# Optimization experiments

Hardware: AMD Instinct MI355X
Metric: run time of the kernel (lower is better)

## Reference

```python
import jax, jax.numpy as jnp
import numpy as np

B, N, D, H, F = 2, 2048, 1024, 16, 4096
E = D // H
EPS = 1e-5

def layer_norm(x, g, b):
    mu = jnp.mean(x, axis=-1, keepdims=True)
    var = jnp.var(x, axis=-1, keepdims=True)
    return (x - mu) * jax.lax.rsqrt(var + EPS) * g + b

def setup_inputs() -> dict:
    key = jax.random.key(0)
    ks = jax.random.split(key, 16)
    s = lambda k, sh, fan: jax.random.normal(k, sh, jnp.float32) * (1.0 / np.sqrt(fan))
    return {
        'x': jax.random.normal(ks[0], (B, N, D), jnp.float32),
        'wq': s(ks[1], (D, D), D), 'bq': jnp.zeros((D,), jnp.float32),
        'wk': s(ks[2], (D, D), D), 'bk': jnp.zeros((D,), jnp.float32),
        'wv': s(ks[3], (D, D), D), 'bv': jnp.zeros((D,), jnp.float32),
        'w1': s(ks[4], (F, D), D), 'b1': jnp.zeros((F,), jnp.float32),
        'ln_mlp_g': jnp.ones((F,), jnp.float32), 'ln_mlp_b': jnp.zeros((F,), jnp.float32),
        'w2': s(ks[5], (D, F), F), 'b2': jnp.zeros((D,), jnp.float32),
        'ln1_g': jnp.ones((D,), jnp.float32), 'ln1_b': jnp.zeros((D,), jnp.float32),
        'ln2_g': jnp.ones((D,), jnp.float32), 'ln2_b': jnp.zeros((D,), jnp.float32),
    }

def reference(x, wq, bq, wk, bk, wv, bv, w1, b1, ln_mlp_g, ln_mlp_b, w2, b2, ln1_g, ln1_b, ln2_g, ln2_b):
    h = layer_norm(x, ln1_g, ln1_b)                       # [B,N,D]
    q = (h @ wq.T + bq).reshape(B, N, H, E).transpose(0, 2, 1, 3)  # [B,H,N,E]
    k = (h @ wk.T + bk).reshape(B, N, H, E).transpose(0, 2, 1, 3)
    v = (h @ wv.T + bv).reshape(B, N, H, E).transpose(0, 2, 1, 3)
    # faithful to source: score = q@k^T / sqrt(1/emb_dim) == q@k^T * sqrt(emb_dim)
    score = jnp.einsum('bhne,bhme->bhnm', q, k) * np.sqrt(D).astype(np.float32)
    causal = jnp.tril(jnp.ones((N, N), bool))
    score = jnp.where(causal[None, None], score, -jnp.inf)
    weight = jax.nn.softmax(score, axis=-1)
    attn = jnp.einsum('bhnm,bhme->bhne', weight, v)       # [B,H,N,E]
    attn = attn.transpose(0, 2, 1, 3).reshape(B, N, D)
    x = x + attn
    h2 = layer_norm(x, ln2_g, ln2_b)
    m = h2 @ w1.T + b1                                    # [B,N,F]
    m = jax.nn.relu(layer_norm(m, ln_mlp_g, ln_mlp_b))
    # faithful: no second residual in the source forward
    return m @ w2.T + b2
```

## Files before the change

kernel.cpp:

```cpp
#include <hip/hip_runtime.h>
#include <cstdint>

typedef __bf16 bf16_t;
typedef bf16_t bf16x8 __attribute__((ext_vector_type(8)));
typedef bf16_t bf16x4 __attribute__((ext_vector_type(4)));
typedef float  floatx4 __attribute__((ext_vector_type(4)));

#define GLD_LDS(g, l) __builtin_amdgcn_global_load_lds( \
    (const __attribute__((address_space(1))) unsigned int*)(g), \
    (__attribute__((address_space(3))) unsigned int*)(l), 16, 0, 0)

#define MFMA_BF16_16x16x32 __builtin_amdgcn_mfma_f32_16x16x32_bf16

__global__ __launch_bounds__(256) void prep(
    const float* __restrict__ wq, const float* __restrict__ wk,
    const float* __restrict__ wv, const float* __restrict__ w1,
    const float* __restrict__ w2, const float* __restrict__ bq,
    const float* __restrict__ bk,
    bf16_t* __restrict__ wqk_hi, bf16_t* __restrict__ wqk_lo,
    bf16_t* __restrict__ wvb, bf16_t* __restrict__ w1b, bf16_t* __restrict__ w2b,
    float* __restrict__ bqk) {
  const int blk = blockIdx.x, tid = threadIdx.x;
  if (blk < 2048) {
    const int qk = blk >> 10;
    const int i  = (blk & 1023) * 256 + tid;
    const float* src = qk ? wk : wq;
    float4 v = ((const float4*)src)[i];
    float f[4] = {v.x, v.y, v.z, v.w};
    bf16x4 h, l;
    #pragma unroll
    for (int j = 0; j < 4; ++j) { h[j] = (bf16_t)f[j]; l[j] = (bf16_t)(f[j] - (float)h[j]); }
    ((bf16x4*)(wqk_hi + qk * 1024 * 1024))[i] = h;
    ((bf16x4*)(wqk_lo + qk * 1024 * 1024))[i] = l;
  } else if (blk < 3072) {
    const int i = (blk - 2048) * 256 + tid;
    float4 v = ((const float4*)wv)[i];
    bf16x4 o; o[0]=(bf16_t)v.x; o[1]=(bf16_t)v.y; o[2]=(bf16_t)v.z; o[3]=(bf16_t)v.w;
    ((bf16x4*)wvb)[i] = o;
  } else if (blk < 7168) {
    const int i = (blk - 3072) * 256 + tid;
    float4 v = ((const float4*)w1)[i];
    bf16x4 o; o[0]=(bf16_t)v.x; o[1]=(bf16_t)v.y; o[2]=(bf16_t)v.z; o[3]=(bf16_t)v.w;
    ((bf16x4*)w1b)[i] = o;
  } else if (blk < 11264) {
    const int i = (blk - 7168) * 256 + tid;
    float4 v = ((const float4*)w2)[i];
    bf16x4 o; o[0]=(bf16_t)v.x; o[1]=(bf16_t)v.y; o[2]=(bf16_t)v.z; o[3]=(bf16_t)v.w;
    ((bf16x4*)w2b)[i] = o;
  } else {
    const int i = (blk - 11264) * 256 + tid;
    if (i < 1024) { bqk[i] = bq[i]; bqk[1024 + i] = bk[i]; }
  }
}


__device__ __forceinline__ void block_sum2(float& s, float& ss, float* red) {
  #pragma unroll
  for (int off = 32; off > 0; off >>= 1) {
    s  += __shfl_down(s, off);
    ss += __shfl_down(ss, off);
  }
  const int wave = threadIdx.x >> 6;
  if ((threadIdx.x & 63) == 0) { red[wave * 2] = s; red[wave * 2 + 1] = ss; }
  __syncthreads();
  s  = red[0] + red[2] + red[4] + red[6];
  ss = red[1] + red[3] + red[5] + red[7];
}

__global__ __launch_bounds__(256) void ln_fwd_split(const float* __restrict__ x,
    const float* __restrict__ g, const float* __restrict__ b,
    bf16_t* __restrict__ out_hi, bf16_t* __restrict__ out_lo) {
  __shared__ float red[8];
  const size_t row = blockIdx.x;
  float4 v = ((const float4*)(x + row * 1024))[threadIdx.x];
  float s  = v.x + v.y + v.z + v.w;
  float ss = v.x*v.x + v.y*v.y + v.z*v.z + v.w*v.w;
  block_sum2(s, ss, red);
  const float mu  = s * (1.f / 1024.f);
  const float var = ss * (1.f / 1024.f) - mu * mu;
  const float rs  = rsqrtf(var + 1e-5f);
  float4 gg = ((const float4*)g)[threadIdx.x];
  float4 bb = ((const float4*)b)[threadIdx.x];
  float f[4];
  f[0] = (v.x - mu) * rs * gg.x + bb.x;
  f[1] = (v.y - mu) * rs * gg.y + bb.y;
  f[2] = (v.z - mu) * rs * gg.z + bb.z;
  f[3] = (v.w - mu) * rs * gg.w + bb.w;
  bf16x4 oh, ol;
  #pragma unroll
  for (int j = 0; j < 4; ++j) {
    oh[j] = (bf16_t)f[j];
    ol[j] = (bf16_t)(f[j] - (float)oh[j]);
  }
  ((bf16x4*)(out_hi + row * 1024))[threadIdx.x] = oh;
  ((bf16x4*)(out_lo + row * 1024))[threadIdx.x] = ol;
}

__global__ __launch_bounds__(256) void resid_ln_fwd(const float* __restrict__ x,
    const float* __restrict__ a, const float* __restrict__ g, const float* __restrict__ b,
    bf16_t* __restrict__ out) {
  __shared__ float red[8];
  const size_t row = blockIdx.x;
  float4 v = ((const float4*)(x + row * 1024))[threadIdx.x];
  float4 av = ((const float4*)(a + row * 1024))[threadIdx.x];
  v.x += av.x; v.y += av.y; v.z += av.z; v.w += av.w;
  float s  = v.x + v.y + v.z + v.w;
  float ss = v.x*v.x + v.y*v.y + v.z*v.z + v.w*v.w;
  block_sum2(s, ss, red);
  const float mu  = s * (1.f / 1024.f);
  const float var = ss * (1.f / 1024.f) - mu * mu;
  const float rs  = rsqrtf(var + 1e-5f);
  float4 gg = ((const float4*)g)[threadIdx.x];
  float4 bb = ((const float4*)b)[threadIdx.x];
  bf16x4 o;
  o[0] = (bf16_t)((v.x - mu) * rs * gg.x + bb.x);
  o[1] = (bf16_t)((v.y - mu) * rs * gg.y + bb.y);
  o[2] = (bf16_t)((v.z - mu) * rs * gg.z + bb.z);
  o[3] = (bf16_t)((v.w - mu) * rs * gg.w + bb.w);
  ((bf16x4*)(out + row * 1024))[threadIdx.x] = o;
}

__global__ __launch_bounds__(256) void ln_relu_inplace(bf16_t* __restrict__ m,
    const float* __restrict__ g, const float* __restrict__ b) {
  __shared__ float red[8];
  const size_t row = blockIdx.x;
  bf16_t* mr = m + row * 4096;
  const int base = threadIdx.x * 16;
  bf16x8 v0 = *(bf16x8*)(mr + base);
  bf16x8 v1 = *(bf16x8*)(mr + base + 8);
  float f[16];
  #pragma unroll
  for (int i = 0; i < 8; ++i) { f[i] = (float)v0[i]; f[8 + i] = (float)v1[i]; }
  float s = 0.f, ss = 0.f;
  #pragma unroll
  for (int i = 0; i < 16; ++i) { s += f[i]; ss += f[i] * f[i]; }
  block_sum2(s, ss, red);
  const float mu  = s * (1.f / 4096.f);
  const float var = ss * (1.f / 4096.f) - mu * mu;
  const float rs  = rsqrtf(var + 1e-5f);
  bf16x8 o0, o1;
  #pragma unroll
  for (int i = 0; i < 16; ++i) {
    float ov = (f[i] - mu) * rs * g[base + i] + b[base + i];
    ov = fmaxf(ov, 0.f);
    if (i < 8) o0[i] = (bf16_t)ov; else o1[i - 8] = (bf16_t)ov;
  }
  *(bf16x8*)(mr + base) = o0;
  *(bf16x8*)(mr + base + 8) = o1;
}

template <int OUT_MODE, int BM>
__global__ __launch_bounds__(256) void gemm_bt(
    const bf16_t* __restrict__ A, const bf16_t* __restrict__ Bw,
    const float* __restrict__ bias, void* __restrict__ Cp,
    int M, int N, int K) {
  constexpr int MI = BM / 32;
  __shared__ bf16_t As[BM * 32];
  __shared__ bf16_t Bs[128 * 32];
  const int tid  = threadIdx.x;
  const int wave = tid >> 6, lane = tid & 63;
  const int quad = lane >> 4, l15 = lane & 15;
  const int m0 = blockIdx.x * BM, n0 = blockIdx.y * 128;
  const int wm = (wave >> 1) * (BM / 2), wn = (wave & 1) * 64;
  const int srowA = wave * (BM / 4) + (lane >> 2);
  const int srowB = wave * 32 + (lane >> 2);
  const int scol = (lane & 3) * 8;

  floatx4 acc[MI][4] = {};

  const bf16_t* Ag = A  + (size_t)(m0 + srowA) * K + scol;
  const bf16_t* Bg = Bw + (size_t)(n0 + srowB) * K + scol;

  for (int k0 = 0; k0 < K; k0 += 32) {
    __syncthreads();
    #pragma unroll
    for (int i = 0; i < BM / 64; ++i)
      GLD_LDS(Ag + (size_t)(i * 16) * K + k0, As + wave * (BM / 4) * 32 + i * 512);
    #pragma unroll
    for (int i = 0; i < 2; ++i)
      GLD_LDS(Bg + (size_t)(i * 16) * K + k0, Bs + wave * 1024 + i * 512);
    __syncthreads();
    bf16x8 af[MI], bfr[4];
    #pragma unroll
    for (int i = 0; i < MI; ++i)
      af[i] = *(const bf16x8*)(As + (wm + i * 16 + l15) * 32 + quad * 8);
    #pragma unroll
    for (int j = 0; j < 4; ++j)
      bfr[j] = *(const bf16x8*)(Bs + (wn + j * 16 + l15) * 32 + quad * 8);
    #pragma unroll
    for (int i = 0; i < MI; ++i)
      #pragma unroll
      for (int j = 0; j < 4; ++j)
        acc[i][j] = MFMA_BF16_16x16x32(af[i], bfr[j], acc[i][j], 0, 0, 0);
  }
  #pragma unroll
  for (int j = 0; j < 4; ++j) {
    const int col = n0 + wn + j * 16 + l15;
    const float bv = bias[col];
    #pragma unroll
    for (int i = 0; i < MI; ++i) {
      #pragma unroll
      for (int r = 0; r < 4; ++r) {
        const int row = m0 + wm + i * 16 + quad * 4 + r;
        const float v = acc[i][j][r] + bv;
        if (OUT_MODE == 0) {
          ((float*)Cp)[(size_t)row * N + col] = v;
        } else if (OUT_MODE == 1) {
          ((bf16_t*)Cp)[(size_t)row * N + col] = (bf16_t)v;
        } else {
          const int b = row >> 11, n = row & 2047;
          const int h = col >> 6, e = col & 63;
          ((bf16_t*)Cp)[(((size_t)((b << 4) + h) * 2048 + n) << 6) + e] = (bf16_t)v;
        }
      }
    }
  }
}

__global__ __launch_bounds__(256) void gemm_qk_split(
    const bf16_t* __restrict__ Ah, const bf16_t* __restrict__ Al,
    const bf16_t* __restrict__ Bh, const bf16_t* __restrict__ Bl,
    const float* __restrict__ bias,
    bf16_t* __restrict__ qhi, bf16_t* __restrict__ qlo,
    bf16_t* __restrict__ khi, bf16_t* __restrict__ klo,
    int M, int N, int K) {
  __shared__ bf16_t Ash[64 * 32];
  __shared__ bf16_t Asl[64 * 32];
  __shared__ bf16_t Bsh[128 * 32];
  __shared__ bf16_t Bsl[128 * 32];
  const int tid  = threadIdx.x;
  const int wave = tid >> 6, lane = tid & 63;
  const int quad = lane >> 4, l15 = lane & 15;
  const int m0 = blockIdx.x * 64, n0 = blockIdx.y * 128;
  const int wm = (wave >> 1) * 32, wn = (wave & 1) * 64;
  const int srowA = wave * 16 + (lane >> 2);
  const int srowB = wave * 32 + (lane >> 2);
  const int scol = (lane & 3) * 8;

  floatx4 acc[2][4] = {};

  const size_t aoff = (size_t)(m0 + srowA) * K + scol;
  const size_t boff = (size_t)(n0 + srowB) * K + scol;

  for (int k0 = 0; k0 < K; k0 += 32) {
    __syncthreads();
    GLD_LDS(Ah + aoff + k0, Ash + wave * 512);
    GLD_LDS(Al + aoff + k0, Asl + wave * 512);
    #pragma unroll
    for (int i = 0; i < 2; ++i) {
      const size_t gb = boff + (size_t)(i * 16) * K + k0;
      GLD_LDS(Bh + gb, Bsh + wave * 1024 + i * 512);
      GLD_LDS(Bl + gb, Bsl + wave * 1024 + i * 512);
    }
    __syncthreads();
    bf16x8 ah[2], al[2], bh[4], bl[4];
    #pragma unroll
    for (int i = 0; i < 2; ++i) {
      const int ro = (wm + i * 16 + l15) * 32 + quad * 8;
      ah[i] = *(const bf16x8*)(Ash + ro);
      al[i] = *(const bf16x8*)(Asl + ro);
    }
    #pragma unroll
    for (int j = 0; j < 4; ++j) {
      const int ro = (wn + j * 16 + l15) * 32 + quad * 8;
      bh[j] = *(const bf16x8*)(Bsh + ro);
      bl[j] = *(const bf16x8*)(Bsl + ro);
    }
    #pragma unroll
    for (int i = 0; i < 2; ++i)
      #pragma unroll
      for (int j = 0; j < 4; ++j) {
        acc[i][j] = MFMA_BF16_16x16x32(ah[i], bh[j], acc[i][j], 0, 0, 0);
        acc[i][j] = MFMA_BF16_16x16x32(ah[i], bl[j], acc[i][j], 0, 0, 0);
        acc[i][j] = MFMA_BF16_16x16x32(al[i], bh[j], acc[i][j], 0, 0, 0);
      }
  }
  #pragma unroll
  for (int j = 0; j < 4; ++j) {
    const int col = n0 + wn + j * 16 + l15;
    const float bv = bias[col];
    const bool isq = col < 1024;
    bf16_t* hib = isq ? qhi : khi;
    bf16_t* lob = isq ? qlo : klo;
    const float scale = isq ? 32.0f : 1.0f;
    const int h = (col >> 6) & 15, e = col & 63;
    #pragma unroll
    for (int i = 0; i < 2; ++i) {
      #pragma unroll
      for (int r = 0; r < 4; ++r) {
        const int row = m0 + wm + i * 16 + quad * 4 + r;
        const int b = row >> 11, n = row & 2047;
        const float c = (acc[i][j][r] + bv) * scale;
        const bf16_t chi = (bf16_t)c;
        const bf16_t clo = (bf16_t)(c - (float)chi);
        const size_t dst = (((size_t)((b << 4) + h) * 2048 + n) << 6) + e;
        hib[dst] = chi;
        lob[dst] = clo;
      }
    }
  }
}

__global__ __launch_bounds__(256) void transpose_v(
    const bf16_t* __restrict__ vhm, bf16_t* __restrict__ vT) {
  __shared__ bf16_t T[64 * 72];
  const int bh = blockIdx.x, n0 = blockIdx.y * 64;
  const int r = threadIdx.x >> 2;
  const int c = (threadIdx.x & 3) * 16;
  const bf16_t* src = vhm + ((size_t)bh * 2048 + n0 + r) * 64 + c;
  bf16x8 a0 = *(const bf16x8*)src;
  bf16x8 a1 = *(const bf16x8*)(src + 8);
  #pragma unroll
  for (int j = 0; j < 8; ++j) {
    T[(c + j) * 72 + r]     = a0[j];
    T[(c + 8 + j) * 72 + r] = a1[j];
  }
  __syncthreads();
  bf16x8 o0 = *(const bf16x8*)(T + r * 72 + c);
  bf16x8 o1 = *(const bf16x8*)(T + r * 72 + c + 8);
  bf16_t* dst = vT + ((size_t)(bh * 64 + r)) * 2048 + n0 + c;
  *(bf16x8*)dst = o0;
  *(bf16x8*)(dst + 8) = o1;
}

__global__ __launch_bounds__(256, 4) void attn_causal(
    const bf16_t* __restrict__ qhi, const bf16_t* __restrict__ qlo,
    const bf16_t* __restrict__ khi, const bf16_t* __restrict__ klo,
    const bf16_t* __restrict__ vT, float* __restrict__ o) {
  __shared__ bf16_t KsH[64 * 72];
  __shared__ bf16_t KsL[64 * 72];
  __shared__ bf16_t Vt[64 * 72];
  __shared__ bf16_t Ps[4][16 * 70];

  const int tid  = threadIdx.x;
  const int wave = tid >> 6, lane = tid & 63;
  const int quad = lane >> 4, l15 = lane & 15;
  const int bh = blockIdx.x;
  const int q0 = (31 - (int)blockIdx.y) * 64;
  const size_t hb = (size_t)bh * 2048;

  const int wmin = q0 + wave * 16;
  const int qrow = wmin + l15;
  bf16x8 qh[2], ql[2];
  {
    const bf16_t* qbh = qhi + ((hb + wmin + l15) << 6) + quad * 8;
    const bf16_t* qbl = qlo + ((hb + wmin + l15) << 6) + quad * 8;
    qh[0] = *(const bf16x8*)qbh;
    qh[1] = *(const bf16x8*)(qbh + 32);
    ql[0] = *(const bf16x8*)qbl;
    ql[1] = *(const bf16x8*)(qbl + 32);
  }

  floatx4 accO[4] = {};
  float m_row = -1e30f;
  float l_row = 0.f;

  const int kr = wave * 16 + (lane >> 3);
  const int kc = (lane & 7) * 8;
  const bf16_t* kgh = khi + ((hb + kr) << 6) + kc;
  const bf16_t* kgl = klo + ((hb + kr) << 6) + kc;
  const bf16_t* vg  = vT + ((size_t)(bh * 64 + kr)) * 2048 + kc;

  bf16x8 pkh0 = *(const bf16x8*)(kgh);
  bf16x8 pkh1 = *(const bf16x8*)(kgh + (8 << 6));
  bf16x8 pkl0 = *(const bf16x8*)(kgl);
  bf16x8 pkl1 = *(const bf16x8*)(kgl + (8 << 6));
  bf16x8 pv0  = *(const bf16x8*)(vg);
  bf16x8 pv1  = *(const bf16x8*)(vg + 8 * 2048);

  const int ntiles = (q0 >> 6) + 1;
  for (int t = 0; t < ntiles; ++t) {
    const int k0 = t * 64;
    __syncthreads();
    *(bf16x8*)(KsH + kr * 72 + kc)       = pkh0;
    *(bf16x8*)(KsH + (kr + 8) * 72 + kc) = pkh1;
    *(bf16x8*)(KsL + kr * 72 + kc)       = pkl0;
    *(bf16x8*)(KsL + (kr + 8) * 72 + kc) = pkl1;
    *(bf16x8*)(Vt  + kr * 72 + kc)       = pv0;
    *(bf16x8*)(Vt  + (kr + 8) * 72 + kc) = pv1;
    if (t + 1 < ntiles) {
      const int koff = (t + 1) << 12;
      pkh0 = *(const bf16x8*)(kgh + koff);
      pkh1 = *(const bf16x8*)(kgh + koff + (8 << 6));
      pkl0 = *(const bf16x8*)(kgl + koff);
      pkl1 = *(const bf16x8*)(kgl + koff + (8 << 6));
      pv0  = *(const bf16x8*)(vg + (t + 1) * 64);
      pv1  = *(const bf16x8*)(vg + (t + 1) * 64 + 8 * 2048);
    }
    __syncthreads();

    const bool needmask = (k0 + 63 > wmin);

    floatx4 sv[4];
    #pragma unroll
    for (int j = 0; j < 4; ++j) {
      const bf16_t* kbh = KsH + (j * 16 + l15) * 72;
      const bf16_t* kbl = KsL + (j * 16 + l15) * 72;
      const bf16x8 kh0 = *(const bf16x8*)(kbh + quad * 8);
      const bf16x8 kh1 = *(const bf16x8*)(kbh + 32 + quad * 8);
      const bf16x8 kl0 = *(const bf16x8*)(kbl + quad * 8);
      const bf16x8 kl1 = *(const bf16x8*)(kbl + 32 + quad * 8);
      floatx4 acc = {};
      acc = MFMA_BF16_16x16x32(kh0, qh[0], acc, 0, 0, 0);
      acc = MFMA_BF16_16x16x32(kh1, qh[1], acc, 0, 0, 0);
      acc = MFMA_BF16_16x16x32(kl0, qh[0], acc, 0, 0, 0);
      acc = MFMA_BF16_16x16x32(kl1, qh[1], acc, 0, 0, 0);
      acc = MFMA_BF16_16x16x32(kh0, ql[0], acc, 0, 0, 0);
      acc = MFMA_BF16_16x16x32(kh1, ql[1], acc, 0, 0, 0);
      sv[j] = acc;
    }

    const int lim = qrow - k0 - quad * 4;
    float mr = -1e30f;
    #pragma unroll
    for (int j = 0; j < 4; ++j)
      #pragma unroll
      for (int r = 0; r < 4; ++r) {
        float x = sv[j][r];
        if (needmask && (j * 16 + r > lim)) x = -1e30f;
        sv[j][r] = x;
        mr = fmaxf(mr, x);
      }
    mr = fmaxf(mr, __shfl_xor(mr, 16));
    mr = fmaxf(mr, __shfl_xor(mr, 32));
    const float mold = m_row;
    const float mnew = fmaxf(mold, mr);
    m_row = mnew;
    float psum = 0.f;
    bf16x4 pb[4];
    #pragma unroll
    for (int j = 0; j < 4; ++j)
      #pragma unroll
      for (int r = 0; r < 4; ++r) {
        const float p = __expf(sv[j][r] - mnew);
        const bf16_t pv = (bf16_t)p;
        psum += (float)pv;
        pb[j][r] = pv;
      }
    {
      bf16_t* pw = &Ps[wave][l15 * 70];
      #pragma unroll
      for (int j = 0; j < 4; ++j)
        *(bf16x4*)(pw + j * 16 + quad * 4) = pb[j];
    }
    psum += __shfl_xor(psum, 16);
    psum += __shfl_xor(psum, 32);
    const float alpha = __expf(mold - mnew);
    l_row = l_row * alpha + psum;
    if (__any(mnew > mold)) {
      #pragma unroll
      for (int r = 0; r < 4; ++r) {
        const float ar = __shfl(alpha, quad * 4 + r);
        #pragma unroll
        for (int j = 0; j < 4; ++j) accO[j][r] *= ar;
      }
    }
    asm volatile("s_waitcnt lgkmcnt(0)" ::: "memory");

    bf16x8 pf[2];
    {
      const bf16_t* pr = &Ps[wave][l15 * 70];
      pf[0] = *(const bf16x8*)(pr + quad * 8);
      pf[1] = *(const bf16x8*)(pr + 32 + quad * 8);
    }
    #pragma unroll
    for (int j = 0; j < 4; ++j) {
      const bf16_t* vb = Vt + (j * 16 + l15) * 72;
      const bf16x8 vf0 = *(const bf16x8*)(vb + quad * 8);
      const bf16x8 vf1 = *(const bf16x8*)(vb + 32 + quad * 8);
      accO[j] = MFMA_BF16_16x16x32(pf[0], vf0, accO[j], 0, 0, 0);
      accO[j] = MFMA_BF16_16x16x32(pf[1], vf1, accO[j], 0, 0, 0);
    }
  }

  const int b = bh >> 4, h = bh & 15;
  #pragma unroll
  for (int r = 0; r < 4; ++r) {
    const float lr = __shfl(l_row, quad * 4 + r);
    const float linv = 1.f / lr;
    const int qr = wmin + quad * 4 + r;
    float* orow = o + ((size_t)(b * 2048) + qr) * 1024 + h * 64;
    #pragma unroll
    for (int j = 0; j < 4; ++j)
      orow[j * 16 + l15] = accO[j][r] * linv;
  }
}


extern "C" void kernel_launch(void* const* d_in, const int* in_sizes, int n_in,
                              void* d_out, int out_size, void* d_ws, size_t ws_size,
                              hipStream_t stream) {
  const float* x        = (const float*)d_in[0];
  const float* wq       = (const float*)d_in[1];
  const float* bq       = (const float*)d_in[2];
  const float* wk       = (const float*)d_in[3];
  const float* bk       = (const float*)d_in[4];
  const float* wv       = (const float*)d_in[5];
  const float* bv       = (const float*)d_in[6];
  const float* w1       = (const float*)d_in[7];
  const float* b1       = (const float*)d_in[8];
  const float* ln_mlp_g = (const float*)d_in[9];
  const float* ln_mlp_b = (const float*)d_in[10];
  const float* w2       = (const float*)d_in[11];
  const float* b2       = (const float*)d_in[12];
  const float* ln1_g    = (const float*)d_in[13];
  const float* ln1_b    = (const float*)d_in[14];
  const float* ln2_g    = (const float*)d_in[15];
  const float* ln2_b    = (const float*)d_in[16];

  char* ws = (char*)d_ws;
  bf16_t* h_hi   = (bf16_t*)(ws);
  bf16_t* h_lo   = (bf16_t*)(ws + (8u  << 20));
  bf16_t* vTb    = (bf16_t*)(ws);
  bf16_t* wqk_hi = (bf16_t*)(ws + (16u << 20));
  bf16_t* wqk_lo = (bf16_t*)(ws + (20u << 20));
  bf16_t* wvb    = (bf16_t*)(ws + (24u << 20));
  float*  bqk    = (float*) (ws + (26u << 20));
  bf16_t* w1b    = (bf16_t*)(ws + (28u << 20));
  bf16_t* w2b    = (bf16_t*)(ws + (36u << 20));
  bf16_t* qhi    = (bf16_t*)(ws + (44u << 20));
  bf16_t* qlo    = (bf16_t*)(ws + (52u << 20));
  bf16_t* khi    = (bf16_t*)(ws + (60u << 20));
  bf16_t* klo    = (bf16_t*)(ws + (68u << 20));
  bf16_t* mbuf   = (bf16_t*)(ws + (44u << 20));
  bf16_t* vhm    = (bf16_t*)(ws + (76u << 20));
  float*  attnb  = (float*) (ws + (84u << 20));
  bf16_t* h2     = (bf16_t*)(ws + (100u << 20));

  prep<<<11268, 256, 0, stream>>>(wq, wk, wv, w1, w2, bq, bk,
                                  wqk_hi, wqk_lo, wvb, w1b, w2b, bqk);

  ln_fwd_split<<<4096, 256, 0, stream>>>(x, ln1_g, ln1_b, h_hi, h_lo);
  gemm_qk_split<<<dim3(64, 16), 256, 0, stream>>>(h_hi, h_lo, wqk_hi, wqk_lo, bqk,
                                                  qhi, qlo, khi, klo, 4096, 2048, 1024);
  gemm_bt<2, 64><<<dim3(64, 8), 256, 0, stream>>>(h_hi, wvb, bv, vhm, 4096, 1024, 1024);
  transpose_v<<<dim3(32, 32), 256, 0, stream>>>(vhm, vTb);
  attn_causal<<<dim3(32, 32), 256, 0, stream>>>(qhi, qlo, khi, klo, vTb, attnb);
  resid_ln_fwd<<<4096, 256, 0, stream>>>(x, attnb, ln2_g, ln2_b, h2);
  gemm_bt<1, 128><<<dim3(32, 32), 256, 0, stream>>>(h2, w1b, b1, mbuf, 4096, 4096, 1024);
  ln_relu_inplace<<<4096, 256, 0, stream>>>(mbuf, ln_mlp_g, ln_mlp_b);
  gemm_bt<0, 64><<<dim3(64, 8), 256, 0, stream>>>(mbuf, w2b, b2, d_out, 4096, 1024, 4096);

  (void)in_sizes; (void)n_in; (void)out_size; (void)ws_size;
}
```

Baseline: 472.8 us.

## Swizzle attention LDS layout, add XCD block remap and MFMA priority hints

Replaces the padded LDS tiles in the attention kernel with XOR-swizzled unpadded layouts. This cuts shared memory per block and raises the occupancy hint from 4 to 5 blocks. It also adds an XCD-aware block index remap to the GEMM kernels to improve L2 locality, and wraps the attention MFMA sections in s_setprio plus a sched_barrier. The swizzle must keep bank conflicts low, and the remap assumes the grid size divides evenly by 8.

```diff
diff --git a/kernel.cpp b/kernel.cpp
--- a/kernel.cpp
+++ b/kernel.cpp
@@ -149,6 +149,15 @@
   *(bf16x8*)(mr + base + 8) = o1;
 }
 
+__device__ __forceinline__ void xcd_swizzle(int& bx, int& by) {
+  const int gx = gridDim.x;
+  const int nwg = gx * gridDim.y;
+  const int flat = by * gx + bx;
+  const int cpx = nwg >> 3;
+  const int swz = (flat & 7) * cpx + (flat >> 3);
+  bx = swz % gx; by = swz / gx;
+}
+
 template <int OUT_MODE, int BM>
 __global__ __launch_bounds__(256) void gemm_bt(
     const bf16_t* __restrict__ A, const bf16_t* __restrict__ Bw,
@@ -160,7 +169,9 @@
   const int tid  = threadIdx.x;
   const int wave = tid >> 6, lane = tid & 63;
   const int quad = lane >> 4, l15 = lane & 15;
-  const int m0 = blockIdx.x * BM, n0 = blockIdx.y * 128;
+  int bx = blockIdx.x, by = blockIdx.y;
+  xcd_swizzle(bx, by);
+  const int m0 = bx * BM, n0 = by * 128;
   const int wm = (wave >> 1) * (BM / 2), wn = (wave & 1) * 64;
   const int srowA = wave * (BM / 4) + (lane >> 2);
   const int srowB = wave * 32 + (lane >> 2);
@@ -231,7 +242,9 @@
   const int tid  = threadIdx.x;
   const int wave = tid >> 6, lane = tid & 63;
   const int quad = lane >> 4, l15 = lane & 15;
-  const int m0 = blockIdx.x * 64, n0 = blockIdx.y * 128;
+  int bx = blockIdx.x, by = blockIdx.y;
+  xcd_swizzle(bx, by);
+  const int m0 = bx * 64, n0 = by * 128;
   const int wm = (wave >> 1) * 32, wn = (wave & 1) * 64;
   const int srowA = wave * 16 + (lane >> 2);
   const int srowB = wave * 32 + (lane >> 2);
@@ -323,14 +336,15 @@
   *(bf16x8*)(dst + 8) = o1;
 }
 
-__global__ __launch_bounds__(256, 4) void attn_causal(
+#define SWZ(row, chunk) (((row) << 6) + ((((chunk) ^ ((row) & 7))) << 3))
+__global__ __launch_bounds__(256, 5) void attn_causal(
     const bf16_t* __restrict__ qhi, const bf16_t* __restrict__ qlo,
     const bf16_t* __restrict__ khi, const bf16_t* __restrict__ klo,
     const bf16_t* __restrict__ vT, float* __restrict__ o) {
-  __shared__ bf16_t KsH[64 * 72];
-  __shared__ bf16_t KsL[64 * 72];
-  __shared__ bf16_t Vt[64 * 72];
-  __shared__ bf16_t Ps[4][16 * 70];
+  __shared__ bf16_t KsH[64 * 64];
+  __shared__ bf16_t KsL[64 * 64];
+  __shared__ bf16_t Vt[64 * 64];
+  __shared__ bf16_t Ps[4][16 * 64];
 
   const int tid  = threadIdx.x;
   const int wave = tid >> 6, lane = tid & 63;
@@ -356,10 +370,10 @@
   float l_row = 0.f;
 
   const int kr = wave * 16 + (lane >> 3);
-  const int kc = (lane & 7) * 8;
-  const bf16_t* kgh = khi + ((hb + kr) << 6) + kc;
-  const bf16_t* kgl = klo + ((hb + kr) << 6) + kc;
-  const bf16_t* vg  = vT + ((size_t)(bh * 64 + kr)) * 2048 + kc;
+  const int kc7 = lane & 7;
+  const bf16_t* kgh = khi + ((hb + kr) << 6) + kc7 * 8;
+  const bf16_t* kgl = klo + ((hb + kr) << 6) + kc7 * 8;
+  const bf16_t* vg  = vT + ((size_t)(bh * 64 + kr)) * 2048 + kc7 * 8;
 
   bf16x8 pkh0 = *(const bf16x8*)(kgh);
   bf16x8 pkh1 = *(const bf16x8*)(kgh + (8 << 6));
@@ -372,12 +386,12 @@
   for (int t = 0; t < ntiles; ++t) {
     const int k0 = t * 64;
     __syncthreads();
-    *(bf16x8*)(KsH + kr * 72 + kc)       = pkh0;
-    *(bf16x8*)(KsH + (kr + 8) * 72 + kc) = pkh1;
-    *(bf16x8*)(KsL + kr * 72 + kc)       = pkl0;
-    *(bf16x8*)(KsL + (kr + 8) * 72 + kc) = pkl1;
-    *(bf16x8*)(Vt  + kr * 72 + kc)       = pv0;
-    *(bf16x8*)(Vt  + (kr + 8) * 72 + kc) = pv1;
+    *(bf16x8*)(KsH + SWZ(kr, kc7))     = pkh0;
+    *(bf16x8*)(KsH + SWZ(kr + 8, kc7)) = pkh1;
+    *(bf16x8*)(KsL + SWZ(kr, kc7))     = pkl0;
+    *(bf16x8*)(KsL + SWZ(kr + 8, kc7)) = pkl1;
+    *(bf16x8*)(Vt  + SWZ(kr, kc7))     = pv0;
+    *(bf16x8*)(Vt  + SWZ(kr + 8, kc7)) = pv1;
     if (t + 1 < ntiles) {
       const int koff = (t + 1) << 12;
       pkh0 = *(const bf16x8*)(kgh + koff);
@@ -392,14 +406,14 @@
     const bool needmask = (k0 + 63 > wmin);
 
     floatx4 sv[4];
+    __builtin_amdgcn_s_setprio(1);
     #pragma unroll
     for (int j = 0; j < 4; ++j) {
-      const bf16_t* kbh = KsH + (j * 16 + l15) * 72;
-      const bf16_t* kbl = KsL + (j * 16 + l15) * 72;
-      const bf16x8 kh0 = *(const bf16x8*)(kbh + quad * 8);
-      const bf16x8 kh1 = *(const bf16x8*)(kbh + 32 + quad * 8);
-      const bf16x8 kl0 = *(const bf16x8*)(kbl + quad * 8);
-      const bf16x8 kl1 = *(const bf16x8*)(kbl + 32 + quad * 8);
+      const int rK = j * 16 + l15;
+      const bf16x8 kh0 = *(const bf16x8*)(KsH + SWZ(rK, quad));
+      const bf16x8 kh1 = *(const bf16x8*)(KsH + SWZ(rK, quad + 4));
+      const bf16x8 kl0 = *(const bf16x8*)(KsL + SWZ(rK, quad));
+      const bf16x8 kl1 = *(const bf16x8*)(KsL + SWZ(rK, quad + 4));
       floatx4 acc = {};
       acc = MFMA_BF16_16x16x32(kh0, qh[0], acc, 0, 0, 0);
       acc = MFMA_BF16_16x16x32(kh1, qh[1], acc, 0, 0, 0);
@@ -409,6 +423,7 @@
       acc = MFMA_BF16_16x16x32(kh1, ql[1], acc, 0, 0, 0);
       sv[j] = acc;
     }
+    __builtin_amdgcn_s_setprio(0);
 
     const int lim = qrow - k0 - quad * 4;
     float mr = -1e30f;
@@ -438,10 +453,10 @@
         pb[j][r] = pv;
       }
     {
-      bf16_t* pw = &Ps[wave][l15 * 70];
+      bf16_t* pw = &Ps[wave][0];
       #pragma unroll
       for (int j = 0; j < 4; ++j)
-        *(bf16x4*)(pw + j * 16 + quad * 4) = pb[j];
+        *(bf16x4*)(pw + SWZ(l15, 2 * j + (quad >> 1)) + (quad & 1) * 4) = pb[j];
     }
     psum += __shfl_xor(psum, 16);
     psum += __shfl_xor(psum, 32);
@@ -456,21 +471,24 @@
       }
     }
     asm volatile("s_waitcnt lgkmcnt(0)" ::: "memory");
+    __builtin_amdgcn_sched_barrier(0);
 
     bf16x8 pf[2];
     {
-      const bf16_t* pr = &Ps[wave][l15 * 70];
-      pf[0] = *(const bf16x8*)(pr + quad * 8);
-      pf[1] = *(const bf16x8*)(pr + 32 + quad * 8);
-    }
+      const bf16_t* pw = &Ps[wave][0];
+      pf[0] = *(const bf16x8*)(pw + SWZ(l15, quad));
+      pf[1] = *(const bf16x8*)(pw + SWZ(l15, quad + 4));
+    }
+    __builtin_amdgcn_s_setprio(1);
     #pragma unroll
     for (int j = 0; j < 4; ++j) {
-      const bf16_t* vb = Vt + (j * 16 + l15) * 72;
-      const bf16x8 vf0 = *(const bf16x8*)(vb + quad * 8);
-      const bf16x8 vf1 = *(const bf16x8*)(vb + 32 + quad * 8);
+      const int rV = j * 16 + l15;
+      const bf16x8 vf0 = *(const bf16x8*)(Vt + SWZ(rV, quad));
+      const bf16x8 vf1 = *(const bf16x8*)(Vt + SWZ(rV, quad + 4));
       accO[j] = MFMA_BF16_16x16x32(pf[0], vf0, accO[j], 0, 0, 0);
       accO[j] = MFMA_BF16_16x16x32(pf[1], vf1, accO[j], 0, 0, 0);
     }
+    __builtin_amdgcn_s_setprio(0);
   }
 
   const int b = bh >> 4, h = bh & 15;
```

Result: slower. 503.6 us (+6.5%).
